# Optimization experiments

Measured on AMD Instinct MI355X. Metric: run time of the kernel, lower is better.

## Reference

```python
import jax, jax.numpy as jnp
import numpy as np
import math

N_COMP = 8          # config.project.shape[1]
REG_TOPK = 4        # config.reg_topk
PROJ_MAX = 7.0      # config.project = linspace(0, 7, 8)
ACC = PROJ_MAX / (N_COMP - 1)  # = 1.0


def _conv(x, w, b, pad):
    y = jax.lax.conv_general_dilated(
        x, w, window_strides=(1, 1), padding=[(pad, pad), (pad, pad)],
        dimension_numbers=("NCHW", "OIHW", "NCHW"))
    return y + b[None, :, None, None]


def setup_inputs() -> dict:
    key = jax.random.key(0)
    ks = jax.random.split(key, 16)
    std = 0.01
    f32 = jnp.float32
    feature = jax.random.normal(ks[0], (8, 256, 100, 152), dtype=f32)
    cls_w = jax.random.normal(ks[1], (4, 256, 256, 3, 3), dtype=f32) * std
    cls_b = jnp.zeros((4, 256), dtype=f32)
    box_w = jax.random.normal(ks[2], (4, 256, 256, 3, 3), dtype=f32) * std
    box_b = jnp.zeros((4, 256), dtype=f32)
    score_w = jax.random.normal(ks[3], (1, 256, 3, 3), dtype=f32) * std
    score_b = jnp.full((1,), -math.log((1 - 0.01) / 0.01), dtype=f32)
    pred_w = jax.random.normal(ks[4], (64, 256, 3, 3), dtype=f32) * std
    pred_b = jnp.zeros((64,), dtype=f32)
    ctn_w = jax.random.normal(ks[5], (1, 256, 3, 3), dtype=f32) * std
    ctn_b = jnp.zeros((1,), dtype=f32)
    conf_w1 = jax.random.normal(ks[6], (64, 48, 1, 1), dtype=f32) * std
    conf_b1 = jnp.zeros((64,), dtype=f32)
    conf_w2 = jax.random.normal(ks[7], (1, 64, 1, 1), dtype=f32) * std
    conf_b2 = jnp.zeros((1,), dtype=f32)
    return dict(feature=feature, cls_w=cls_w, cls_b=cls_b, box_w=box_w, box_b=box_b,
                score_w=score_w, score_b=score_b, pred_w=pred_w, pred_b=pred_b,
                ctn_w=ctn_w, ctn_b=ctn_b, conf_w1=conf_w1, conf_b1=conf_b1,
                conf_w2=conf_w2, conf_b2=conf_b2)


def reference(feature, cls_w, cls_b, box_w, box_b, score_w, score_b,
              pred_w, pred_b, ctn_w, ctn_b, conf_w1, conf_b1, conf_w2, conf_b2):
    x = feature
    for i in range(4):
        x = jax.nn.relu(_conv(x, cls_w[i], cls_b[i], 1))
    cls_score = _conv(x, score_w, score_b, 1)          # (N,1,H,W)
    # bbox subnet
    y = feature
    for i in range(4):
        y = jax.nn.relu(_conv(y, box_w[i], box_b[i], 1))
    bbox_pred = _conv(y, pred_w, pred_b, 1)            # (N,64,H,W)
    ctn = _conv(y, ctn_w, ctn_b, 1)                    # (N,1,H,W)

    N, C, H, W = bbox_pred.shape
    # rows = N*H*W*4 (4 box sides), 16 = 2*n_component per side
    flat = bbox_pred.transpose(0, 2, 3, 1).reshape(-1, 2 * N_COMP)
    logit = flat[:, :N_COMP]
    lstd = flat[:, N_COMP:]
    prob = jax.nn.softmax(logit, axis=1)               # (rows, n)
    sigma = jnp.exp(lstd)                              # (rows, n)
    proj = jnp.arange(N_COMP, dtype=flat.dtype) * ACC  # linspace(0, 7, 8)
    inv = 1.0 / (sigma * jnp.asarray(np.sqrt(2.0), flat.dtype))  # (rows, n)
    # Normal(mean=proj_i, std=sigma_i).cdf(proj_j +/- acc)
    diff = proj[None, None, :] - proj[None, :, None]   # (1, n_i, n_j) = z_j - mean_i
    cdf_hi = 0.5 * (1.0 + jax.lax.erf((diff + ACC) * inv[:, :, None]))
    cdf_lo = 0.5 * (1.0 + jax.lax.erf((diff - ACC) * inv[:, :, None]))
    pmf = jnp.sum((cdf_hi - cdf_lo) * prob[:, :, None], axis=1)  # (rows, n)

    toppmf, idx = jax.lax.top_k(pmf, REG_TOPK)         # (rows, k)
    toplstd = jnp.take_along_axis(lstd, idx, axis=1)
    topprob = jnp.take_along_axis(prob, idx, axis=1)

    def tochw(t):  # (rows,k) -> (N, 4*k, H, W)
        return t.reshape(N, H, W, -1).transpose(0, 3, 1, 2)

    stat = jnp.concatenate([tochw(toplstd), tochw(topprob), tochw(toppmf)], axis=1)  # (N,48,H,W)
    h = jax.nn.relu(_conv(stat, conf_w1, conf_b1, 0))
    quality = jax.nn.sigmoid(_conv(h, conf_w2, conf_b2, 0))  # (N,1,H,W)

    cls_out = jax.nn.sigmoid(cls_score) * quality
    pred_cls = cls_out.transpose(0, 2, 3, 1).reshape(N, -1, 1)
    pred_reg = bbox_pred.transpose(0, 2, 3, 1).reshape(N, -1, 4 * 2 * N_COMP)
    pred_ctn = ctn.transpose(0, 2, 3, 1).reshape(N, -1, 1)
    return (pred_cls, pred_reg, pred_ctn)
```

## Files before the change

kernel.cpp:

```cpp
#include <hip/hip_runtime.h>

typedef unsigned short u16;
typedef _Float16 f16;
typedef __attribute__((ext_vector_type(4))) float f32x4;
typedef __attribute__((ext_vector_type(8))) _Float16 f16x8;
typedef __attribute__((ext_vector_type(8))) unsigned short u16x8;

#define NIMG 8
#define HH 100
#define WW 152
#define HP 102
#define WP 154
#define NPIX (NIMG*HH*WW)
#define ACT_ELEMS ((size_t)NIMG*HP*WP*256)
#define ACT_BYTES (ACT_ELEMS*2)

__device__ __forceinline__ u16 f2h(float x){
    f16 h = (f16)x;
    return __builtin_bit_cast(u16, h);
}

__device__ __forceinline__ void g2l16(const u16* g, u16* l){
    __builtin_amdgcn_global_load_lds((const __attribute__((address_space(1))) unsigned int*)g,
                                     (__attribute__((address_space(3))) unsigned int*)l, 16, 0, 0);
}

__global__ void zero_borders(u16* A, u16* B){
    int id = blockIdx.x*256 + threadIdx.x;
    int ch = id & 31; int t = id >> 5;
    int pb = t % 508; int nimg = t / 508;
    int hp, wp;
    if (pb < 154)      { hp = 0;            wp = pb; }
    else if (pb < 308) { hp = 101;          wp = pb - 154; }
    else if (pb < 408) { hp = pb - 308 + 1; wp = 0; }
    else               { hp = pb - 408 + 1; wp = 153; }
    size_t off = ((size_t)((nimg*HP + hp)*WP + wp))*256 + ch*8;
    u16x8 z = {};
    *(u16x8*)(A+off) = z; *(u16x8*)(B+off) = z;
}

__global__ void feat2act(const float* __restrict__ F, u16* __restrict__ D){
    __shared__ float t[64][65];
    int bid = blockIdx.x;
    int wb = bid % 3; bid /= 3;
    int cb = bid & 3; bid >>= 2;
    int h = bid % 100; int nimg = bid / 100;
    int c0 = cb*64, w0 = wb*64;
    int tid = threadIdx.x;
    int cl = tid >> 6;
    int wl = tid & 63;
    #pragma unroll
    for (int rr=0; rr<16; ++rr){
        int c = rr*4 + cl;
        int w = w0 + wl;
        float v = 0.f;
        if (w < WW) v = F[ ((size_t)((nimg*256 + c0 + c)*HH + h))*WW + w ];
        t[c][wl] = v;
    }
    __syncthreads();
    int wl2 = tid >> 6;
    int cl2 = tid & 63;
    #pragma unroll
    for (int rr=0; rr<16; ++rr){
        int w = rr*4 + wl2;
        if (w0 + w < WW){
            size_t dst = ((size_t)((nimg*HP + h + 1)*WP + (w0 + w + 1)))*256 + c0 + cl2;
            D[dst] = f2h(t[cl2][w]);
        }
    }
}

__global__ void wt_tower(const float* __restrict__ src, u16* __restrict__ d){
    int idx = blockIdx.x*256 + threadIdx.x;
    int ci = idx & 255; int t = idx >> 8;
    int co = t & 255; t >>= 8;
    int tap = t % 9; int l = t / 9;
    d[idx] = f2h(src[ ((size_t)((l*256+co)*256+ci))*9 + tap ]);
}
__global__ void wt_predctn(const float* __restrict__ pw, const float* __restrict__ cw,
                           u16* __restrict__ d){
    int idx = blockIdx.x*256 + threadIdx.x;
    int ci = idx & 255; int co = (idx>>8) & 127; int tap = idx >> 15;
    float v = 0.f;
    if (co < 64)       v = pw[ ((size_t)(co*256+ci))*9 + tap ];
    else if (co == 64) v = cw[ (size_t)ci*9 + tap ];
    d[idx] = f2h(v);
}
__global__ void wt_score(const float* __restrict__ sw, u16* __restrict__ d){
    int idx = blockIdx.x*256 + threadIdx.x;
    int ci = idx & 255; int co = (idx>>8) & 127; int tap = idx >> 15;
    d[idx] = f2h((co == 0) ? sw[ (size_t)ci*9 + tap ] : 0.f);
}
__global__ void prep_bias(const float* pb, const float* cb, const float* sb, float* bpc, float* bsc){
    int i = threadIdx.x;
    bpc[i] = (i < 64) ? pb[i] : ((i == 64) ? cb[0] : 0.f);
    bsc[i] = (i == 0) ? sb[0] : 0.f;
}

template<int MODE>
__global__ __launch_bounds__(256, 2) void conv3x3_k(
    const u16* __restrict__ Ah, const u16* __restrict__ Wh,
    const float* __restrict__ bias,
    u16* __restrict__ Oh,
    float* __restrict__ O1, float* __restrict__ O2,
    int NB, int COUTP)
{
    __shared__ u16 lds[32768];
    const int tid  = threadIdx.x;
    const int lane = tid & 63;
    const int wave = tid >> 6;

    int nwg = gridDim.x;
    int bid = blockIdx.x;
    int qq  = nwg >> 3;
    int swz = (bid & 7)*qq + (bid >> 3);
    int nblk = swz % NB;
    int mblk = swz / NB;
    int nimg = mblk / 125;
    int rem  = mblk - nimg*125;
    int ht   = rem / 5;
    int wt5  = rem - ht*5;
    int h0 = ht*4, w0 = wt5*32;
    int co0 = nblk*128;

    int aoff[4], boff[4];
    #pragma unroll
    for (int it=0; it<4; ++it){
        int s = it*256 + tid;
        int p = s >> 3, ch = s & 7;
        int chs = ch ^ (p & 7);
        int i = p >> 5, j = p & 31;
        aoff[it] = ((nimg*HP + h0 + i)*WP + (w0 + j))*256 + chs*8;
        boff[it] = (co0 + p)*256 + chs*8;
    }
    const int ldst = wave*512;

    const int r  = lane & 15;
    const int q4 = lane >> 4;
    const int c0k = ((q4    ) ^ (r & 7)) * 8;
    const int c1k = ((q4 + 4) ^ (r & 7)) * 8;
    const int wm = wave >> 1, wn = wave & 1;
    const int aBase = (wm*64 + r)*64;
    const int bBase = 8192 + (wn*64 + r)*64;

    f32x4 acc[4][4];
    #pragma unroll
    for (int m=0;m<4;m++)
        #pragma unroll
        for (int n=0;n<4;n++)
            acc[m][n] = (f32x4)0.0f;

    auto stage = [&](int t, int b){
        int tap = t >> 2, kb = t & 3;
        int kh = tap/3, kw = tap - kh*3;
        int adel = (kh*WP + kw)*256 + kb*64;
        int bdel = tap*COUTP*256 + kb*64;
        u16* L = lds + b*16384;
        #pragma unroll
        for (int it=0; it<4; ++it)
            g2l16(Ah + aoff[it] + adel, L +        it*2048 + ldst);
        #pragma unroll
        for (int it=0; it<4; ++it)
            g2l16(Wh + boff[it] + bdel, L + 8192 + it*2048 + ldst);
    };

    stage(0, 0);
    stage(1, 1);
    asm volatile("s_waitcnt vmcnt(8)" ::: "memory");
    __builtin_amdgcn_s_barrier();

    for (int t=0; t<36; ++t){
        int b = t & 1;
        const u16* L = lds + b*16384;
        f16x8 a0[4], a1[4], b0[4], b1[4];
        #pragma unroll
        for (int m=0;m<4;m++){
            a0[m] = *(const f16x8*)(L + aBase + m*1024 + c0k);
            a1[m] = *(const f16x8*)(L + aBase + m*1024 + c1k);
            b0[m] = *(const f16x8*)(L + bBase + m*1024 + c0k);
            b1[m] = *(const f16x8*)(L + bBase + m*1024 + c1k);
        }
        asm volatile("s_waitcnt lgkmcnt(0)" ::: "memory");
        __builtin_amdgcn_s_barrier();
        __builtin_amdgcn_sched_barrier(0);
        if (t < 34) stage(t+2, b);
        __builtin_amdgcn_s_setprio(1);
        #pragma unroll
        for (int n=0;n<4;n++){
            #pragma unroll
            for (int m=0;m<4;m++){
                acc[m][n] = __builtin_amdgcn_mfma_f32_16x16x32_f16(a0[m], b0[n], acc[m][n], 0,0,0);
                acc[m][n] = __builtin_amdgcn_mfma_f32_16x16x32_f16(a1[m], b1[n], acc[m][n], 0,0,0);
            }
        }
        __builtin_amdgcn_s_setprio(0);
        __builtin_amdgcn_sched_barrier(0);
        if (t < 34) { asm volatile("s_waitcnt vmcnt(8)" ::: "memory"); }
        else        { asm volatile("s_waitcnt vmcnt(0)" ::: "memory"); }
        __builtin_amdgcn_s_barrier();
    }

    float bcol[4];
    #pragma unroll
    for (int n=0;n<4;n++) bcol[n] = bias[co0 + wn*64 + n*16 + r];

    if (MODE == 0){
        #pragma unroll
        for (int m=0;m<4;m++)
            #pragma unroll
            for (int n=0;n<4;n++)
                #pragma unroll
                for (int jj=0;jj<4;jj++){
                    float v = fmaxf(acc[m][n][jj] + bcol[n], 0.f);
                    int p = wm*64 + m*16 + q4*4 + jj;
                    int c = wn*64 + n*16 + r;
                    lds[p*128 + c] = f2h(v);
                }
        __syncthreads();
        #pragma unroll
        for (int it=0; it<8; ++it){
            int s = it*256 + tid;
            int p = s >> 4, chh = s & 15;
            int i = p >> 5, j = p & 31;
            if (w0 + j < WW){
                size_t dst = ((size_t)((nimg*HP + h0 + i + 1)*WP + (w0 + j + 1)))*256 + co0 + chh*8;
                *(u16x8*)(Oh + dst) = *(const u16x8*)(lds + p*128 + chh*8);
            }
        }
    } else {
        #pragma unroll
        for (int m=0;m<4;m++)
            #pragma unroll
            for (int n=0;n<4;n++)
                #pragma unroll
                for (int jj=0;jj<4;jj++){
                    float v = acc[m][n][jj] + bcol[n];
                    int p = wm*64 + m*16 + q4*4 + jj;
                    int c = co0 + wn*64 + n*16 + r;
                    int i = p >> 5, j = p & 31;
                    if (w0 + j < WW){
                        int pix = nimg*(HH*WW) + (h0+i)*WW + (w0+j);
                        if (MODE == 1){
                            if (c < 64)       O1[(size_t)pix*64 + c] = v;
                            else if (c == 64) O2[pix] = v;
                        } else {
                            if (c == 0) O1[pix] = v;
                        }
                    }
                }
    }
}

__global__ __launch_bounds__(256) void fuse_stat(
    const float* __restrict__ bbox, const float* __restrict__ cls_score,
    const float* __restrict__ w1, const float* __restrict__ b1,
    const float* __restrict__ w2, const float* __restrict__ b2,
    float* __restrict__ pred_cls)
{
    __shared__ float sstat[48][256];
    int tid = threadIdx.x;
    int pix = blockIdx.x*256 + tid;
    if (pix >= NPIX) return;
    const f32x4* row4 = (const f32x4*)(bbox + (size_t)pix*64);
    for (int g=0; g<4; ++g){
        f32x4 v0 = row4[g*4+0], v1 = row4[g*4+1], v2 = row4[g*4+2], v3 = row4[g*4+3];
        float lg[8], ls[8];
        #pragma unroll
        for (int k=0;k<4;k++){ lg[k]=v0[k]; lg[4+k]=v1[k]; ls[k]=v2[k]; ls[4+k]=v3[k]; }
        float m = lg[0];
        #pragma unroll
        for (int k=1;k<8;k++) m = fmaxf(m, lg[k]);
        float e[8], s = 0.f;
        #pragma unroll
        for (int k=0;k<8;k++){ e[k] = expf(lg[k]-m); s += e[k]; }
        float isum = 1.0f/s;
        float prob[8];
        #pragma unroll
        for (int k=0;k<8;k++) prob[k] = e[k]*isum;
        float pmf[8];
        #pragma unroll
        for (int k=0;k<8;k++) pmf[k] = 0.f;
        #pragma unroll
        for (int i=0;i<8;i++){
            float invi = 1.0f/(expf(ls[i]) * 1.41421356237309515f);
            float pi = prob[i];
            #pragma unroll
            for (int j=0;j<8;j++){
                float d = (float)(j - i);
                pmf[j] = fmaf(0.5f*(erff((d+1.0f)*invi) - erff((d-1.0f)*invi)), pi, pmf[j]);
            }
        }
        int used = 0;
        #pragma unroll
        for (int t=0;t<4;t++){
            float bv = -3.0e38f; int bi = 0;
            #pragma unroll
            for (int j=0;j<8;j++){
                bool ok = (((used>>j)&1)==0) && (pmf[j] > bv);
                bv = ok ? pmf[j] : bv;
                bi = ok ? j : bi;
            }
            used |= (1<<bi);
            float sl=0.f, sp=0.f;
            #pragma unroll
            for (int j=0;j<8;j++){ if (j==bi){ sl=ls[j]; sp=prob[j]; } }
            sstat[g*4+t][tid]    = sl;
            sstat[16+g*4+t][tid] = sp;
            sstat[32+g*4+t][tid] = bv;
        }
    }
    float q = b2[0];
    for (int u=0; u<64; ++u){
        float h = b1[u];
        #pragma unroll
        for (int c=0;c<48;c++) h = fmaf(sstat[c][tid], w1[u*48+c], h);
        q = fmaf(fmaxf(h,0.f), w2[u], q);
    }
    float quality = 1.0f/(1.0f+expf(-q));
    float cs = cls_score[pix];
    pred_cls[pix] = quality/(1.0f+expf(-cs));
}

extern "C" void kernel_launch(void* const* d_in, const int* in_sizes, int n_in,
                              void* d_out, int out_size, void* d_ws, size_t ws_size,
                              hipStream_t stream) {
    (void)in_sizes; (void)n_in; (void)out_size;
    const float* feature = (const float*)d_in[0];
    const float* cls_w   = (const float*)d_in[1];
    const float* cls_b   = (const float*)d_in[2];
    const float* box_w   = (const float*)d_in[3];
    const float* box_b   = (const float*)d_in[4];
    const float* score_w = (const float*)d_in[5];
    const float* score_b = (const float*)d_in[6];
    const float* pred_w  = (const float*)d_in[7];
    const float* pred_b  = (const float*)d_in[8];
    const float* ctn_w   = (const float*)d_in[9];
    const float* ctn_b   = (const float*)d_in[10];
    const float* conf_w1 = (const float*)d_in[11];
    const float* conf_b1 = (const float*)d_in[12];
    const float* conf_w2 = (const float*)d_in[13];
    const float* conf_b2 = (const float*)d_in[14];

    float* out      = (float*)d_out;
    float* pred_cls = out;
    float* pred_reg = out + NPIX;
    float* pred_ctn = out + NPIX + (size_t)NPIX*64;

    char* ws = (char*)d_ws;
    size_t off = 0;
    auto alloc = [&](size_t b){ size_t rr = off; off += (b + 255) & ~(size_t)255; return rr; };
    u16* aA = (u16*)(ws + alloc(ACT_BYTES));
    u16* aB = (u16*)(ws + alloc(ACT_BYTES));
    const size_t TWR = (size_t)4*9*256*256;
    const size_t HDW = (size_t)9*128*256;
    u16* wCls = (u16*)(ws + alloc(TWR*2));
    u16* wBox = (u16*)(ws + alloc(TWR*2));
    u16* wSc  = (u16*)(ws + alloc(HDW*2));
    u16* wPc  = (u16*)(ws + alloc(HDW*2));
    float* bPc = (float*)(ws + alloc(128*4));
    float* bSc = (float*)(ws + alloc(128*4));
    float* clsScore = (float*)(ws + alloc((size_t)NPIX*4));
    if (ws_size < off) return;

    dim3 B(256);
    zero_borders<<<508, B, 0, stream>>>(aA, aB);
    wt_tower<<<9216, B, 0, stream>>>(cls_w, wCls);
    wt_tower<<<9216, B, 0, stream>>>(box_w, wBox);
    wt_score<<<1152, B, 0, stream>>>(score_w, wSc);
    wt_predctn<<<1152, B, 0, stream>>>(pred_w, ctn_w, wPc);
    prep_bias<<<1, 128, 0, stream>>>(pred_b, ctn_b, score_b, bPc, bSc);

    const size_t LW = (size_t)9*256*256;
    feat2act<<<9600, B, 0, stream>>>(feature, aA);
    conv3x3_k<0><<<2000, B, 0, stream>>>(aA, wCls+0*LW, cls_b+0*256, aB, nullptr, nullptr, 2, 256);
    conv3x3_k<0><<<2000, B, 0, stream>>>(aB, wCls+1*LW, cls_b+1*256, aA, nullptr, nullptr, 2, 256);
    conv3x3_k<0><<<2000, B, 0, stream>>>(aA, wCls+2*LW, cls_b+2*256, aB, nullptr, nullptr, 2, 256);
    conv3x3_k<0><<<2000, B, 0, stream>>>(aB, wCls+3*LW, cls_b+3*256, aA, nullptr, nullptr, 2, 256);
    conv3x3_k<2><<<1000, B, 0, stream>>>(aA, wSc, bSc, nullptr, clsScore, nullptr, 1, 128);
    feat2act<<<9600, B, 0, stream>>>(feature, aB);
    conv3x3_k<0><<<2000, B, 0, stream>>>(aB, wBox+0*LW, box_b+0*256, aA, nullptr, nullptr, 2, 256);
    conv3x3_k<0><<<2000, B, 0, stream>>>(aA, wBox+1*LW, box_b+1*256, aB, nullptr, nullptr, 2, 256);
    conv3x3_k<0><<<2000, B, 0, stream>>>(aB, wBox+2*LW, box_b+2*256, aA, nullptr, nullptr, 2, 256);
    conv3x3_k<0><<<2000, B, 0, stream>>>(aA, wBox+3*LW, box_b+3*256, aB, nullptr, nullptr, 2, 256);
    conv3x3_k<1><<<1000, B, 0, stream>>>(aB, wPc, bPc, nullptr, pred_reg, pred_ctn, 1, 128);
    fuse_stat<<<475, B, 0, stream>>>(pred_reg, clsScore, conf_w1, conf_b1, conf_w2, conf_b2, pred_cls);
}
```

Baseline: 1.420 ms.

## Load conv weights straight to registers and trim padded head output channels

The conv kernel no longer stages weight tiles through LDS. Each wave now loads its B fragments from global memory into registers, double-buffered a step ahead. The head convolutions get specialised tiling: 16 output channels for the score head and 80 for pred+ctn instead of 128, with each wave covering 32 pixels, which cuts the wasted MFMA work on padded channels. LDS use halves, but the tower convs now read weights redundantly per wave from global or L2, adding register pressure and load latency on the main path.

```diff
diff --git a/kernel.cpp b/kernel.cpp
--- a/kernel.cpp
+++ b/kernel.cpp
@@ -80,7 +80,8 @@
 __global__ void wt_predctn(const float* __restrict__ pw, const float* __restrict__ cw,
                            u16* __restrict__ d){
     int idx = blockIdx.x*256 + threadIdx.x;
-    int ci = idx & 255; int co = (idx>>8) & 127; int tap = idx >> 15;
+    int ci = idx & 255; int t = idx >> 8;
+    int co = t % 80; int tap = t / 80;
     float v = 0.f;
     if (co < 64)       v = pw[ ((size_t)(co*256+ci))*9 + tap ];
     else if (co == 64) v = cw[ (size_t)ci*9 + tap ];
@@ -88,7 +89,8 @@
 }
 __global__ void wt_score(const float* __restrict__ sw, u16* __restrict__ d){
     int idx = blockIdx.x*256 + threadIdx.x;
-    int ci = idx & 255; int co = (idx>>8) & 127; int tap = idx >> 15;
+    int ci = idx & 255; int t = idx >> 8;
+    int co = t & 15; int tap = t >> 4;
     d[idx] = f2h((co == 0) ? sw[ (size_t)ci*9 + tap ] : 0.f);
 }
 __global__ void prep_bias(const float* pb, const float* cb, const float* sb, float* bpc, float* bsc){
@@ -99,13 +101,17 @@
 
 template<int MODE>
 __global__ __launch_bounds__(256, 2) void conv3x3_k(
-    const u16* __restrict__ Ah, const u16* __restrict__ Wh,
+    const u16* __restrict__ Ain, const u16* __restrict__ W,
     const float* __restrict__ bias,
     u16* __restrict__ Oh,
     float* __restrict__ O1, float* __restrict__ O2,
     int NB, int COUTP)
 {
-    __shared__ u16 lds[32768];
+    constexpr int MR = (MODE==0) ? 4 : 2;
+    constexpr int NR = (MODE==0) ? 4 : ((MODE==1) ? 5 : 1);
+    constexpr int VMN = 4 + 2*NR;
+
+    __shared__ u16 lds[16384];
     const int tid  = threadIdx.x;
     const int lane = tid & 63;
     const int wave = tid >> 6;
@@ -121,9 +127,8 @@
     int ht   = rem / 5;
     int wt5  = rem - ht*5;
     int h0 = ht*4, w0 = wt5*32;
-    int co0 = nblk*128;
-
-    int aoff[4], boff[4];
+
+    int aoff[4];
     #pragma unroll
     for (int it=0; it<4; ++it){
         int s = it*256 + tid;
@@ -131,7 +136,6 @@
         int chs = ch ^ (p & 7);
         int i = p >> 5, j = p & 31;
         aoff[it] = ((nimg*HP + h0 + i)*WP + (w0 + j))*256 + chs*8;
-        boff[it] = (co0 + p)*256 + chs*8;
     }
     const int ldst = wave*512;
 
@@ -139,76 +143,92 @@
     const int q4 = lane >> 4;
     const int c0k = ((q4    ) ^ (r & 7)) * 8;
     const int c1k = ((q4 + 4) ^ (r & 7)) * 8;
-    const int wm = wave >> 1, wn = wave & 1;
-    const int aBase = (wm*64 + r)*64;
-    const int bBase = 8192 + (wn*64 + r)*64;
-
-    f32x4 acc[4][4];
-    #pragma unroll
-    for (int m=0;m<4;m++)
-        #pragma unroll
-        for (int n=0;n<4;n++)
+    int wm, wn;
+    if (MODE == 0){ wm = wave >> 1; wn = wave & 1; } else { wm = wave; wn = 0; }
+    const int aBase = (wm*(MR*16) + r)*64;
+    const int cobase = (MODE==0) ? (nblk*128 + wn*64) : 0;
+
+    int bvo[NR];
+    #pragma unroll
+    for (int n=0;n<NR;n++) bvo[n] = (cobase + n*16 + r)*256 + q4*8;
+
+    f32x4 acc[MR][NR];
+    #pragma unroll
+    for (int m=0;m<MR;m++)
+        #pragma unroll
+        for (int n=0;n<NR;n++)
             acc[m][n] = (f32x4)0.0f;
 
     auto stage = [&](int t, int b){
         int tap = t >> 2, kb = t & 3;
         int kh = tap/3, kw = tap - kh*3;
         int adel = (kh*WP + kw)*256 + kb*64;
-        int bdel = tap*COUTP*256 + kb*64;
-        u16* L = lds + b*16384;
+        u16* L = lds + b*8192;
         #pragma unroll
         for (int it=0; it<4; ++it)
-            g2l16(Ah + aoff[it] + adel, L +        it*2048 + ldst);
-        #pragma unroll
-        for (int it=0; it<4; ++it)
-            g2l16(Wh + boff[it] + bdel, L + 8192 + it*2048 + ldst);
+            g2l16(Ain + aoff[it] + adel, L + it*2048 + ldst);
     };
+    auto loadB = [&](int t, f16x8 (&d)[NR][2]){
+        int tap = t >> 2, kb = t & 3;
+        int base = tap*COUTP*256 + kb*64;
+        #pragma unroll
+        for (int n=0;n<NR;n++){
+            d[n][0] = *(const f16x8*)(W + base + bvo[n]);
+            d[n][1] = *(const f16x8*)(W + base + bvo[n] + 32);
+        }
+    };
+
+    f16x8 bA[NR][2], bB[NR][2];
 
     stage(0, 0);
     stage(1, 1);
-    asm volatile("s_waitcnt vmcnt(8)" ::: "memory");
+    loadB(0, bA);
+    asm volatile("s_waitcnt vmcnt(%0)" :: "i"(VMN) : "memory");
     __builtin_amdgcn_s_barrier();
 
-    for (int t=0; t<36; ++t){
-        int b = t & 1;
-        const u16* L = lds + b*16384;
-        f16x8 a0[4], a1[4], b0[4], b1[4];
-        #pragma unroll
-        for (int m=0;m<4;m++){
-            a0[m] = *(const f16x8*)(L + aBase + m*1024 + c0k);
-            a1[m] = *(const f16x8*)(L + aBase + m*1024 + c1k);
-            b0[m] = *(const f16x8*)(L + bBase + m*1024 + c0k);
-            b1[m] = *(const f16x8*)(L + bBase + m*1024 + c1k);
+    auto step = [&](int t, int b, f16x8 (&use)[NR][2], f16x8 (&nxt)[NR][2]){
+        const u16* L = lds + b*8192;
+        f16x8 af[MR][2];
+        #pragma unroll
+        for (int m=0;m<MR;m++){
+            af[m][0] = *(const f16x8*)(L + aBase + m*1024 + c0k);
+            af[m][1] = *(const f16x8*)(L + aBase + m*1024 + c1k);
         }
         asm volatile("s_waitcnt lgkmcnt(0)" ::: "memory");
         __builtin_amdgcn_s_barrier();
         __builtin_amdgcn_sched_barrier(0);
         if (t < 34) stage(t+2, b);
+        if (t < 35) loadB(t+1, nxt);
         __builtin_amdgcn_s_setprio(1);
         #pragma unroll
-        for (int n=0;n<4;n++){
-            #pragma unroll
-            for (int m=0;m<4;m++){
-                acc[m][n] = __builtin_amdgcn_mfma_f32_16x16x32_f16(a0[m], b0[n], acc[m][n], 0,0,0);
-                acc[m][n] = __builtin_amdgcn_mfma_f32_16x16x32_f16(a1[m], b1[n], acc[m][n], 0,0,0);
+        for (int n=0;n<NR;n++){
+            #pragma unroll
+            for (int m=0;m<MR;m++){
+                acc[m][n] = __builtin_amdgcn_mfma_f32_16x16x32_f16(af[m][0], use[n][0], acc[m][n], 0,0,0);
+                acc[m][n] = __builtin_amdgcn_mfma_f32_16x16x32_f16(af[m][1], use[n][1], acc[m][n], 0,0,0);
             }
         }
         __builtin_amdgcn_s_setprio(0);
         __builtin_amdgcn_sched_barrier(0);
-        if (t < 34) { asm volatile("s_waitcnt vmcnt(8)" ::: "memory"); }
-        else        { asm volatile("s_waitcnt vmcnt(0)" ::: "memory"); }
+        asm volatile("s_waitcnt vmcnt(%0)" :: "i"(VMN) : "memory");
         __builtin_amdgcn_s_barrier();
-    }
-
-    float bcol[4];
-    #pragma unroll
-    for (int n=0;n<4;n++) bcol[n] = bias[co0 + wn*64 + n*16 + r];
+    };
+
+    #pragma unroll 1
+    for (int tt=0; tt<36; tt+=2){
+        step(tt,   0, bA, bB);
+        step(tt+1, 1, bB, bA);
+    }
+
+    float bcol[NR];
+    #pragma unroll
+    for (int n=0;n<NR;n++) bcol[n] = bias[cobase + n*16 + r];
 
     if (MODE == 0){
         #pragma unroll
-        for (int m=0;m<4;m++)
-            #pragma unroll
-            for (int n=0;n<4;n++)
+        for (int m=0;m<MR;m++)
+            #pragma unroll
+            for (int n=0;n<NR;n++)
                 #pragma unroll
                 for (int jj=0;jj<4;jj++){
                     float v = fmaxf(acc[m][n][jj] + bcol[n], 0.f);
@@ -223,20 +243,20 @@
             int p = s >> 4, chh = s & 15;
             int i = p >> 5, j = p & 31;
             if (w0 + j < WW){
-                size_t dst = ((size_t)((nimg*HP + h0 + i + 1)*WP + (w0 + j + 1)))*256 + co0 + chh*8;
+                size_t dst = ((size_t)((nimg*HP + h0 + i + 1)*WP + (w0 + j + 1)))*256 + nblk*128 + chh*8;
                 *(u16x8*)(Oh + dst) = *(const u16x8*)(lds + p*128 + chh*8);
             }
         }
     } else {
         #pragma unroll
-        for (int m=0;m<4;m++)
-            #pragma unroll
-            for (int n=0;n<4;n++)
+        for (int m=0;m<MR;m++)
+            #pragma unroll
+            for (int n=0;n<NR;n++)
                 #pragma unroll
                 for (int jj=0;jj<4;jj++){
                     float v = acc[m][n][jj] + bcol[n];
-                    int p = wm*64 + m*16 + q4*4 + jj;
-                    int c = co0 + wn*64 + n*16 + r;
+                    int p = wm*32 + m*16 + q4*4 + jj;
+                    int c = n*16 + r;
                     int i = p >> 5, j = p & 31;
                     if (w0 + j < WW){
                         int pix = nimg*(HH*WW) + (h0+i)*WW + (w0+j);
@@ -352,11 +372,10 @@
     u16* aA = (u16*)(ws + alloc(ACT_BYTES));
     u16* aB = (u16*)(ws + alloc(ACT_BYTES));
     const size_t TWR = (size_t)4*9*256*256;
-    const size_t HDW = (size_t)9*128*256;
     u16* wCls = (u16*)(ws + alloc(TWR*2));
     u16* wBox = (u16*)(ws + alloc(TWR*2));
-    u16* wSc  = (u16*)(ws + alloc(HDW*2));
-    u16* wPc  = (u16*)(ws + alloc(HDW*2));
+    u16* wSc  = (u16*)(ws + alloc((size_t)9*16*256*2));
+    u16* wPc  = (u16*)(ws + alloc((size_t)9*80*256*2));
     float* bPc = (float*)(ws + alloc(128*4));
     float* bSc = (float*)(ws + alloc(128*4));
     float* clsScore = (float*)(ws + alloc((size_t)NPIX*4));
@@ -366,8 +385,8 @@
     zero_borders<<<508, B, 0, stream>>>(aA, aB);
     wt_tower<<<9216, B, 0, stream>>>(cls_w, wCls);
     wt_tower<<<9216, B, 0, stream>>>(box_w, wBox);
-    wt_score<<<1152, B, 0, stream>>>(score_w, wSc);
-    wt_predctn<<<1152, B, 0, stream>>>(pred_w, ctn_w, wPc);
+    wt_score<<<144, B, 0, stream>>>(score_w, wSc);
+    wt_predctn<<<720, B, 0, stream>>>(pred_w, ctn_w, wPc);
     prep_bias<<<1, 128, 0, stream>>>(pred_b, ctn_b, score_b, bPc, bSc);
 
     const size_t LW = (size_t)9*256*256;
@@ -376,12 +395,12 @@
     conv3x3_k<0><<<2000, B, 0, stream>>>(aB, wCls+1*LW, cls_b+1*256, aA, nullptr, nullptr, 2, 256);
     conv3x3_k<0><<<2000, B, 0, stream>>>(aA, wCls+2*LW, cls_b+2*256, aB, nullptr, nullptr, 2, 256);
     conv3x3_k<0><<<2000, B, 0, stream>>>(aB, wCls+3*LW, cls_b+3*256, aA, nullptr, nullptr, 2, 256);
-    conv3x3_k<2><<<1000, B, 0, stream>>>(aA, wSc, bSc, nullptr, clsScore, nullptr, 1, 128);
+    conv3x3_k<2><<<1000, B, 0, stream>>>(aA, wSc, bSc, nullptr, clsScore, nullptr, 1, 16);
     feat2act<<<9600, B, 0, stream>>>(feature, aB);
     conv3x3_k<0><<<2000, B, 0, stream>>>(aB, wBox+0*LW, box_b+0*256, aA, nullptr, nullptr, 2, 256);
     conv3x3_k<0><<<2000, B, 0, stream>>>(aA, wBox+1*LW, box_b+1*256, aB, nullptr, nullptr, 2, 256);
     conv3x3_k<0><<<2000, B, 0, stream>>>(aB, wBox+2*LW, box_b+2*256, aA, nullptr, nullptr, 2, 256);
     conv3x3_k<0><<<2000, B, 0, stream>>>(aA, wBox+3*LW, box_b+3*256, aB, nullptr, nullptr, 2, 256);
-    conv3x3_k<1><<<1000, B, 0, stream>>>(aB, wPc, bPc, nullptr, pred_reg, pred_ctn, 1, 128);
+    conv3x3_k<1><<<1000, B, 0, stream>>>(aB, wPc, bPc, nullptr, pred_reg, pred_ctn, 1, 80);
     fuse_stat<<<475, B, 0, stream>>>(pred_reg, clsScore, conf_w1, conf_b1, conf_w2, conf_b2, pred_cls);
 }
```

After: 2.864 ms. +101.7%, slower.

## Load a shared halo tile once per channel block and reuse it across taps

Applied to the files above, without the earlier changes.

The 3x3 conv kernel now stages a 10x34-pixel halo of activations into LDS once per 64-channel block and reads all nine tap windows from it, instead of reloading a shifted activation tile from global memory for every tap. Each workgroup grows to 512 threads covering 8x32 output pixels, and only the weight tiles stay double-buffered per tap. The aim is to cut redundant activation traffic and issue fewer global-to-LDS loads per MFMA. In exchange, LDS use per block rises, the grid wastes some work on the partial last row of tiles, rows are clamped at the bottom, and the activation buffers get extra slack space to absorb reads past the end.

```diff
diff --git a/kernel.cpp b/kernel.cpp
--- a/kernel.cpp
+++ b/kernel.cpp
@@ -14,6 +14,10 @@
 #define NPIX (NIMG*HH*WW)
 #define ACT_ELEMS ((size_t)NIMG*HP*WP*256)
 #define ACT_BYTES (ACT_ELEMS*2)
+
+#define HALO_U16 22528
+#define BBUF_U16 8192
+#define LDS_U16  38912
 
 __device__ __forceinline__ u16 f2h(float x){
     f16 h = (f16)x;
@@ -98,14 +102,13 @@
 }
 
 template<int MODE>
-__global__ __launch_bounds__(256, 2) void conv3x3_k(
-    const u16* __restrict__ Ah, const u16* __restrict__ Wh,
+__global__ __launch_bounds__(512, 2) void conv3x3_k(
+    const u16* __restrict__ Ain, const u16* __restrict__ W,
     const float* __restrict__ bias,
-    u16* __restrict__ Oh,
-    float* __restrict__ O1, float* __restrict__ O2,
+    u16* __restrict__ Oh, float* __restrict__ O1, float* __restrict__ O2,
     int NB, int COUTP)
 {
-    __shared__ u16 lds[32768];
+    __shared__ u16 lds[LDS_U16];
     const int tid  = threadIdx.x;
     const int lane = tid & 63;
     const int wave = tid >> 6;
@@ -116,32 +119,39 @@
     int swz = (bid & 7)*qq + (bid >> 3);
     int nblk = swz % NB;
     int mblk = swz / NB;
-    int nimg = mblk / 125;
-    int rem  = mblk - nimg*125;
+    int nimg = mblk / 65;
+    int rem  = mblk - nimg*65;
     int ht   = rem / 5;
     int wt5  = rem - ht*5;
-    int h0 = ht*4, w0 = wt5*32;
+    int h0 = ht*8, w0 = wt5*32;
     int co0 = nblk*128;
 
-    int aoff[4], boff[4];
-    #pragma unroll
-    for (int it=0; it<4; ++it){
-        int s = it*256 + tid;
+    int hsrc[6];
+    #pragma unroll
+    for (int it=0; it<6; ++it){
+        int s = it*512 + tid;
         int p = s >> 3, ch = s & 7;
         int chs = ch ^ (p & 7);
-        int i = p >> 5, j = p & 31;
-        aoff[it] = ((nimg*HP + h0 + i)*WP + (w0 + j))*256 + chs*8;
-        boff[it] = (co0 + p)*256 + chs*8;
-    }
-    const int ldst = wave*512;
+        int hh = p / 34, ww = p - hh*34;
+        int row = h0 + hh; if (row > 101) row = 101;
+        hsrc[it] = ((nimg*HP + row)*WP + (w0 + ww))*256 + chs*8;
+    }
+    int bsrc[2];
+    #pragma unroll
+    for (int it=0; it<2; ++it){
+        int s = it*512 + tid;
+        int p = s >> 3, ch = s & 7;
+        int chs = ch ^ (p & 7);
+        bsrc[it] = (co0 + p)*256 + chs*8;
+    }
+    const int wofs = wave*512;
 
     const int r  = lane & 15;
     const int q4 = lane >> 4;
-    const int c0k = ((q4    ) ^ (r & 7)) * 8;
-    const int c1k = ((q4 + 4) ^ (r & 7)) * 8;
-    const int wm = wave >> 1, wn = wave & 1;
-    const int aBase = (wm*64 + r)*64;
-    const int bBase = 8192 + (wn*64 + r)*64;
+    const int mg = wave >> 1;
+    const int wn = wave & 1;
+    const int laneHBase = mg*68 + r;
+    const int bRead = (wn*64 + r)*64 + (q4 ^ (r & 7))*8;
 
     f32x4 acc[4][4];
     #pragma unroll
@@ -150,52 +160,75 @@
         for (int n=0;n<4;n++)
             acc[m][n] = (f32x4)0.0f;
 
-    auto stage = [&](int t, int b){
-        int tap = t >> 2, kb = t & 3;
-        int kh = tap/3, kw = tap - kh*3;
-        int adel = (kh*WP + kw)*256 + kb*64;
-        int bdel = tap*COUTP*256 + kb*64;
-        u16* L = lds + b*16384;
-        #pragma unroll
-        for (int it=0; it<4; ++it)
-            g2l16(Ah + aoff[it] + adel, L +        it*2048 + ldst);
-        #pragma unroll
-        for (int it=0; it<4; ++it)
-            g2l16(Wh + boff[it] + bdel, L + 8192 + it*2048 + ldst);
+    auto stageHalo = [&](int kb){
+        int kofs = kb*64;
+        u16* L = lds + wofs;
+        #pragma unroll
+        for (int it=0; it<5; ++it)
+            g2l16(Ain + hsrc[it] + kofs, L + it*4096);
+        if (tid < 160) g2l16(Ain + hsrc[5] + kofs, L + 5*4096);
     };
-
-    stage(0, 0);
-    stage(1, 1);
-    asm volatile("s_waitcnt vmcnt(8)" ::: "memory");
+    auto stageB = [&](int tap2, int kb2, int buf){
+        int wb = tap2*COUTP*256 + kb2*64;
+        u16* L = lds + HALO_U16 + buf*BBUF_U16 + wofs;
+        #pragma unroll
+        for (int it=0; it<2; ++it)
+            g2l16(W + wb + bsrc[it], L + it*4096);
+    };
+
+    stageHalo(0);
+    stageB(0, 0, 0);
+    stageB(1, 0, 1);
+    asm volatile("s_waitcnt vmcnt(2)" ::: "memory");
     __builtin_amdgcn_s_barrier();
 
+    #pragma unroll 1
     for (int t=0; t<36; ++t){
-        int b = t & 1;
-        const u16* L = lds + b*16384;
-        f16x8 a0[4], a1[4], b0[4], b1[4];
-        #pragma unroll
-        for (int m=0;m<4;m++){
-            a0[m] = *(const f16x8*)(L + aBase + m*1024 + c0k);
-            a1[m] = *(const f16x8*)(L + aBase + m*1024 + c1k);
-            b0[m] = *(const f16x8*)(L + bBase + m*1024 + c0k);
-            b1[m] = *(const f16x8*)(L + bBase + m*1024 + c1k);
+        int kb  = t/9;
+        int tap = t - kb*9;
+        int kh  = tap/3;
+        int kw  = tap - kh*3;
+        int hp  = laneHBase + kh*34 + kw;
+        int aA  = hp*64  + (q4 ^ (hp  & 7))*8;
+        int hp2 = hp + 34;
+        int aB  = hp2*64 + (q4 ^ (hp2 & 7))*8;
+        const u16* Lb = lds + HALO_U16 + (t & 1)*BBUF_U16;
+
+        f16x8 af[4][2], bf[4][2];
+        af[0][0] = *(const f16x8*)(lds + aA);
+        af[0][1] = *(const f16x8*)(lds + (aA ^ 32));
+        af[1][0] = *(const f16x8*)(lds + aA + 1024);
+        af[1][1] = *(const f16x8*)(lds + (aA ^ 32) + 1024);
+        af[2][0] = *(const f16x8*)(lds + aB);
+        af[2][1] = *(const f16x8*)(lds + (aB ^ 32));
+        af[3][0] = *(const f16x8*)(lds + aB + 1024);
+        af[3][1] = *(const f16x8*)(lds + (aB ^ 32) + 1024);
+        #pragma unroll
+        for (int n=0;n<4;n++){
+            bf[n][0] = *(const f16x8*)(Lb + bRead + n*1024);
+            bf[n][1] = *(const f16x8*)(Lb + (bRead ^ 32) + n*1024);
         }
         asm volatile("s_waitcnt lgkmcnt(0)" ::: "memory");
         __builtin_amdgcn_s_barrier();
         __builtin_amdgcn_sched_barrier(0);
-        if (t < 34) stage(t+2, b);
+        if (tap == 8 && kb < 3) stageHalo(kb+1);
+        if (t < 34){
+            int tn = t + 2;
+            int kbn = tn/9;
+            stageB(tn - kbn*9, kbn, t & 1);
+        }
         __builtin_amdgcn_s_setprio(1);
         #pragma unroll
         for (int n=0;n<4;n++){
             #pragma unroll
             for (int m=0;m<4;m++){
-                acc[m][n] = __builtin_amdgcn_mfma_f32_16x16x32_f16(a0[m], b0[n], acc[m][n], 0,0,0);
-                acc[m][n] = __builtin_amdgcn_mfma_f32_16x16x32_f16(a1[m], b1[n], acc[m][n], 0,0,0);
+                acc[m][n] = __builtin_amdgcn_mfma_f32_16x16x32_f16(af[m][0], bf[n][0], acc[m][n], 0,0,0);
+                acc[m][n] = __builtin_amdgcn_mfma_f32_16x16x32_f16(af[m][1], bf[n][1], acc[m][n], 0,0,0);
             }
         }
         __builtin_amdgcn_s_setprio(0);
         __builtin_amdgcn_sched_barrier(0);
-        if (t < 34) { asm volatile("s_waitcnt vmcnt(8)" ::: "memory"); }
+        if (t < 34) { asm volatile("s_waitcnt vmcnt(2)" ::: "memory"); }
         else        { asm volatile("s_waitcnt vmcnt(0)" ::: "memory"); }
         __builtin_amdgcn_s_barrier();
     }
@@ -212,19 +245,19 @@
                 #pragma unroll
                 for (int jj=0;jj<4;jj++){
                     float v = fmaxf(acc[m][n][jj] + bcol[n], 0.f);
-                    int p = wm*64 + m*16 + q4*4 + jj;
+                    int p = mg*64 + m*16 + q4*4 + jj;
                     int c = wn*64 + n*16 + r;
-                    lds[p*128 + c] = f2h(v);
+                    lds[p*132 + c] = f2h(v);
                 }
         __syncthreads();
         #pragma unroll
         for (int it=0; it<8; ++it){
-            int s = it*256 + tid;
+            int s = it*512 + tid;
             int p = s >> 4, chh = s & 15;
             int i = p >> 5, j = p & 31;
-            if (w0 + j < WW){
+            if (h0 + i < HH && w0 + j < WW){
                 size_t dst = ((size_t)((nimg*HP + h0 + i + 1)*WP + (w0 + j + 1)))*256 + co0 + chh*8;
-                *(u16x8*)(Oh + dst) = *(const u16x8*)(lds + p*128 + chh*8);
+                *(u16x8*)(Oh + dst) = *(const u16x8*)(lds + p*132 + chh*8);
             }
         }
     } else {
@@ -235,10 +268,10 @@
                 #pragma unroll
                 for (int jj=0;jj<4;jj++){
                     float v = acc[m][n][jj] + bcol[n];
-                    int p = wm*64 + m*16 + q4*4 + jj;
-                    int c = co0 + wn*64 + n*16 + r;
+                    int p = mg*64 + m*16 + q4*4 + jj;
+                    int c = wn*64 + n*16 + r;
                     int i = p >> 5, j = p & 31;
-                    if (w0 + j < WW){
+                    if (h0 + i < HH && w0 + j < WW){
                         int pix = nimg*(HH*WW) + (h0+i)*WW + (w0+j);
                         if (MODE == 1){
                             if (c < 64)       O1[(size_t)pix*64 + c] = v;
@@ -349,8 +382,8 @@
     char* ws = (char*)d_ws;
     size_t off = 0;
     auto alloc = [&](size_t b){ size_t rr = off; off += (b + 255) & ~(size_t)255; return rr; };
-    u16* aA = (u16*)(ws + alloc(ACT_BYTES));
-    u16* aB = (u16*)(ws + alloc(ACT_BYTES));
+    u16* aA = (u16*)(ws + alloc(ACT_BYTES + 65536));
+    u16* aB = (u16*)(ws + alloc(ACT_BYTES + 65536));
     const size_t TWR = (size_t)4*9*256*256;
     const size_t HDW = (size_t)9*128*256;
     u16* wCls = (u16*)(ws + alloc(TWR*2));
@@ -371,17 +404,18 @@
     prep_bias<<<1, 128, 0, stream>>>(pred_b, ctn_b, score_b, bPc, bSc);
 
     const size_t LW = (size_t)9*256*256;
+    dim3 CB(512);
     feat2act<<<9600, B, 0, stream>>>(feature, aA);
-    conv3x3_k<0><<<2000, B, 0, stream>>>(aA, wCls+0*LW, cls_b+0*256, aB, nullptr, nullptr, 2, 256);
-    conv3x3_k<0><<<2000, B, 0, stream>>>(aB, wCls+1*LW, cls_b+1*256, aA, nullptr, nullptr, 2, 256);
-    conv3x3_k<0><<<2000, B, 0, stream>>>(aA, wCls+2*LW, cls_b+2*256, aB, nullptr, nullptr, 2, 256);
-    conv3x3_k<0><<<2000, B, 0, stream>>>(aB, wCls+3*LW, cls_b+3*256, aA, nullptr, nullptr, 2, 256);
-    conv3x3_k<2><<<1000, B, 0, stream>>>(aA, wSc, bSc, nullptr, clsScore, nullptr, 1, 128);
+    conv3x3_k<0><<<1040, CB, 0, stream>>>(aA, wCls+0*LW, cls_b+0*256, aB, nullptr, nullptr, 2, 256);
+    conv3x3_k<0><<<1040, CB, 0, stream>>>(aB, wCls+1*LW, cls_b+1*256, aA, nullptr, nullptr, 2, 256);
+    conv3x3_k<0><<<1040, CB, 0, stream>>>(aA, wCls+2*LW, cls_b+2*256, aB, nullptr, nullptr, 2, 256);
+    conv3x3_k<0><<<1040, CB, 0, stream>>>(aB, wCls+3*LW, cls_b+3*256, aA, nullptr, nullptr, 2, 256);
+    conv3x3_k<2><<<520, CB, 0, stream>>>(aA, wSc, bSc, nullptr, clsScore, nullptr, 1, 128);
     feat2act<<<9600, B, 0, stream>>>(feature, aB);
-    conv3x3_k<0><<<2000, B, 0, stream>>>(aB, wBox+0*LW, box_b+0*256, aA, nullptr, nullptr, 2, 256);
-    conv3x3_k<0><<<2000, B, 0, stream>>>(aA, wBox+1*LW, box_b+1*256, aB, nullptr, nullptr, 2, 256);
-    conv3x3_k<0><<<2000, B, 0, stream>>>(aB, wBox+2*LW, box_b+2*256, aA, nullptr, nullptr, 2, 256);
-    conv3x3_k<0><<<2000, B, 0, stream>>>(aA, wBox+3*LW, box_b+3*256, aB, nullptr, nullptr, 2, 256);
-    conv3x3_k<1><<<1000, B, 0, stream>>>(aB, wPc, bPc, nullptr, pred_reg, pred_ctn, 1, 128);
+    conv3x3_k<0><<<1040, CB, 0, stream>>>(aB, wBox+0*LW, box_b+0*256, aA, nullptr, nullptr, 2, 256);
+    conv3x3_k<0><<<1040, CB, 0, stream>>>(aA, wBox+1*LW, box_b+1*256, aB, nullptr, nullptr, 2, 256);
+    conv3x3_k<0><<<1040, CB, 0, stream>>>(aB, wBox+2*LW, box_b+2*256, aA, nullptr, nullptr, 2, 256);
+    conv3x3_k<0><<<1040, CB, 0, stream>>>(aA, wBox+3*LW, box_b+3*256, aB, nullptr, nullptr, 2, 256);
+    conv3x3_k<1><<<520, CB, 0, stream>>>(aB, wPc, bPc, nullptr, pred_reg, pred_ctn, 1, 128);
     fuse_stat<<<475, B, 0, stream>>>(pred_reg, clsScore, conf_w1, conf_b1, conf_w2, conf_b2, pred_cls);
 }
```

Result: slower. 1.957 ms (+37.9%).

## Batch cls and box tower convs into joint launches; trim head MFMA tiles

Applied to the files above, without the earlier changes.

The cls and box towers now run together: each tower layer is one 4000-block launch whose blocks pick cls or box operands by index, using four activation buffers instead of two. Feature conversion writes both tower inputs in a single pass, and the weight transposes are merged into one launch. The head convs (score and pred/ctn) use narrower accumulator tiles (1 or 5 column fragments instead of 4) so padded output channels are not computed. The intent is to cut launch count, fill the GPU better in each launch and drop wasted MFMA work in the heads, at the cost of doubled activation workspace.

```diff
diff --git a/kernel.cpp b/kernel.cpp
--- a/kernel.cpp
+++ b/kernel.cpp
@@ -25,7 +25,7 @@
                                      (__attribute__((address_space(3))) unsigned int*)l, 16, 0, 0);
 }
 
-__global__ void zero_borders(u16* A, u16* B){
+__global__ void zero_borders(u16* A, u16* B, u16* C, u16* D){
     int id = blockIdx.x*256 + threadIdx.x;
     int ch = id & 31; int t = id >> 5;
     int pb = t % 508; int nimg = t / 508;
@@ -37,9 +37,10 @@
     size_t off = ((size_t)((nimg*HP + hp)*WP + wp))*256 + ch*8;
     u16x8 z = {};
     *(u16x8*)(A+off) = z; *(u16x8*)(B+off) = z;
-}
-
-__global__ void feat2act(const float* __restrict__ F, u16* __restrict__ D){
+    *(u16x8*)(C+off) = z; *(u16x8*)(D+off) = z;
+}
+
+__global__ void feat2act(const float* __restrict__ F, u16* __restrict__ D1, u16* __restrict__ D2){
     __shared__ float t[64][65];
     int bid = blockIdx.x;
     int wb = bid % 3; bid /= 3;
@@ -64,14 +65,21 @@
     for (int rr=0; rr<16; ++rr){
         int w = rr*4 + wl2;
         if (w0 + w < WW){
+            u16 h16 = f2h(t[cl2][w]);
             size_t dst = ((size_t)((nimg*HP + h + 1)*WP + (w0 + w + 1)))*256 + c0 + cl2;
-            D[dst] = f2h(t[cl2][w]);
-        }
-    }
-}
-
-__global__ void wt_tower(const float* __restrict__ src, u16* __restrict__ d){
-    int idx = blockIdx.x*256 + threadIdx.x;
+            D1[dst] = h16;
+            D2[dst] = h16;
+        }
+    }
+}
+
+__global__ void wt_tower(const float* __restrict__ srcC, const float* __restrict__ srcB,
+                         u16* __restrict__ dC, u16* __restrict__ dB){
+    int gidx = blockIdx.x*256 + threadIdx.x;
+    const int HALF = 4*9*256*256;
+    const float* src = (gidx < HALF) ? srcC : srcB;
+    u16* d           = (gidx < HALF) ? dC : dB;
+    int idx = (gidx < HALF) ? gidx : gidx - HALF;
     int ci = idx & 255; int t = idx >> 8;
     int co = t & 255; t >>= 8;
     int tap = t % 9; int l = t / 9;
@@ -99,12 +107,16 @@
 
 template<int MODE>
 __global__ __launch_bounds__(256, 2) void conv3x3_k(
-    const u16* __restrict__ Ah, const u16* __restrict__ Wh,
-    const float* __restrict__ bias,
-    u16* __restrict__ Oh,
+    const u16* __restrict__ Ain0, const u16* __restrict__ Ain1,
+    const u16* __restrict__ W0,  const u16* __restrict__ W1,
+    const float* __restrict__ bias0, const float* __restrict__ bias1,
+    u16* __restrict__ Oh0, u16* __restrict__ Oh1,
     float* __restrict__ O1, float* __restrict__ O2,
-    int NB, int COUTP)
+    int nPerTower, int NB, int COUTP)
 {
+    constexpr int MR = (MODE==0) ? 4 : 2;
+    constexpr int NR = (MODE==0) ? 4 : ((MODE==1) ? 5 : 1);
+
     __shared__ u16 lds[32768];
     const int tid  = threadIdx.x;
     const int lane = tid & 63;
@@ -114,8 +126,16 @@
     int bid = blockIdx.x;
     int qq  = nwg >> 3;
     int swz = (bid & 7)*qq + (bid >> 3);
-    int nblk = swz % NB;
-    int mblk = swz / NB;
+    int tower = (swz >= nPerTower) ? 1 : 0;
+    int id = swz - tower*nPerTower;
+
+    const u16* Ain    = tower ? Ain1  : Ain0;
+    const u16* W      = tower ? W1    : W0;
+    const float* bias = tower ? bias1 : bias0;
+    u16* Oh           = tower ? Oh1   : Oh0;
+
+    int nblk = id % NB;
+    int mblk = id / NB;
     int nimg = mblk / 125;
     int rem  = mblk - nimg*125;
     int ht   = rem / 5;
@@ -139,15 +159,16 @@
     const int q4 = lane >> 4;
     const int c0k = ((q4    ) ^ (r & 7)) * 8;
     const int c1k = ((q4 + 4) ^ (r & 7)) * 8;
-    const int wm = wave >> 1, wn = wave & 1;
-    const int aBase = (wm*64 + r)*64;
+    int wm, wn;
+    if (MODE == 0){ wm = wave >> 1; wn = wave & 1; } else { wm = wave; wn = 0; }
+    const int aBase = (wm*(MR*16) + r)*64;
     const int bBase = 8192 + (wn*64 + r)*64;
 
-    f32x4 acc[4][4];
+    f32x4 acc[MR][NR];
     #pragma unroll
-    for (int m=0;m<4;m++)
-        #pragma unroll
-        for (int n=0;n<4;n++)
+    for (int m=0;m<MR;m++)
+        #pragma unroll
+        for (int n=0;n<NR;n++)
             acc[m][n] = (f32x4)0.0f;
 
     auto stage = [&](int t, int b){
@@ -158,10 +179,10 @@
         u16* L = lds + b*16384;
         #pragma unroll
         for (int it=0; it<4; ++it)
-            g2l16(Ah + aoff[it] + adel, L +        it*2048 + ldst);
+            g2l16(Ain + aoff[it] + adel, L +        it*2048 + ldst);
         #pragma unroll
         for (int it=0; it<4; ++it)
-            g2l16(Wh + boff[it] + bdel, L + 8192 + it*2048 + ldst);
+            g2l16(W + bdel + boff[it], L + 8192 + it*2048 + ldst);
     };
 
     stage(0, 0);
@@ -172,13 +193,16 @@
     for (int t=0; t<36; ++t){
         int b = t & 1;
         const u16* L = lds + b*16384;
-        f16x8 a0[4], a1[4], b0[4], b1[4];
-        #pragma unroll
-        for (int m=0;m<4;m++){
+        f16x8 a0[MR], a1[MR], b0[NR], b1[NR];
+        #pragma unroll
+        for (int m=0;m<MR;m++){
             a0[m] = *(const f16x8*)(L + aBase + m*1024 + c0k);
             a1[m] = *(const f16x8*)(L + aBase + m*1024 + c1k);
-            b0[m] = *(const f16x8*)(L + bBase + m*1024 + c0k);
-            b1[m] = *(const f16x8*)(L + bBase + m*1024 + c1k);
+        }
+        #pragma unroll
+        for (int n=0;n<NR;n++){
+            b0[n] = *(const f16x8*)(L + bBase + n*1024 + c0k);
+            b1[n] = *(const f16x8*)(L + bBase + n*1024 + c1k);
         }
         asm volatile("s_waitcnt lgkmcnt(0)" ::: "memory");
         __builtin_amdgcn_s_barrier();
@@ -186,9 +210,9 @@
         if (t < 34) stage(t+2, b);
         __builtin_amdgcn_s_setprio(1);
         #pragma unroll
-        for (int n=0;n<4;n++){
-            #pragma unroll
-            for (int m=0;m<4;m++){
+        for (int n=0;n<NR;n++){
+            #pragma unroll
+            for (int m=0;m<MR;m++){
                 acc[m][n] = __builtin_amdgcn_mfma_f32_16x16x32_f16(a0[m], b0[n], acc[m][n], 0,0,0);
                 acc[m][n] = __builtin_amdgcn_mfma_f32_16x16x32_f16(a1[m], b1[n], acc[m][n], 0,0,0);
             }
@@ -200,15 +224,15 @@
         __builtin_amdgcn_s_barrier();
     }
 
-    float bcol[4];
+    float bcol[NR];
     #pragma unroll
-    for (int n=0;n<4;n++) bcol[n] = bias[co0 + wn*64 + n*16 + r];
+    for (int n=0;n<NR;n++) bcol[n] = bias[co0 + wn*64 + n*16 + r];
 
     if (MODE == 0){
         #pragma unroll
-        for (int m=0;m<4;m++)
-            #pragma unroll
-            for (int n=0;n<4;n++)
+        for (int m=0;m<MR;m++)
+            #pragma unroll
+            for (int n=0;n<NR;n++)
                 #pragma unroll
                 for (int jj=0;jj<4;jj++){
                     float v = fmaxf(acc[m][n][jj] + bcol[n], 0.f);
@@ -229,14 +253,14 @@
         }
     } else {
         #pragma unroll
-        for (int m=0;m<4;m++)
-            #pragma unroll
-            for (int n=0;n<4;n++)
+        for (int m=0;m<MR;m++)
+            #pragma unroll
+            for (int n=0;n<NR;n++)
                 #pragma unroll
                 for (int jj=0;jj<4;jj++){
                     float v = acc[m][n][jj] + bcol[n];
-                    int p = wm*64 + m*16 + q4*4 + jj;
-                    int c = co0 + wn*64 + n*16 + r;
+                    int p = wm*32 + m*16 + q4*4 + jj;
+                    int c = n*16 + r;
                     int i = p >> 5, j = p & 31;
                     if (w0 + j < WW){
                         int pix = nimg*(HH*WW) + (h0+i)*WW + (w0+j);
@@ -349,8 +373,10 @@
     char* ws = (char*)d_ws;
     size_t off = 0;
     auto alloc = [&](size_t b){ size_t rr = off; off += (b + 255) & ~(size_t)255; return rr; };
-    u16* aA = (u16*)(ws + alloc(ACT_BYTES));
-    u16* aB = (u16*)(ws + alloc(ACT_BYTES));
+    u16* aA = (u16*)(ws + alloc(ACT_BYTES + 65536));
+    u16* aB = (u16*)(ws + alloc(ACT_BYTES + 65536));
+    u16* aC = (u16*)(ws + alloc(ACT_BYTES + 65536));
+    u16* aD = (u16*)(ws + alloc(ACT_BYTES + 65536));
     const size_t TWR = (size_t)4*9*256*256;
     const size_t HDW = (size_t)9*128*256;
     u16* wCls = (u16*)(ws + alloc(TWR*2));
@@ -363,25 +389,19 @@
     if (ws_size < off) return;
 
     dim3 B(256);
-    zero_borders<<<508, B, 0, stream>>>(aA, aB);
-    wt_tower<<<9216, B, 0, stream>>>(cls_w, wCls);
-    wt_tower<<<9216, B, 0, stream>>>(box_w, wBox);
+    zero_borders<<<508, B, 0, stream>>>(aA, aB, aC, aD);
+    wt_tower<<<18432, B, 0, stream>>>(cls_w, box_w, wCls, wBox);
     wt_score<<<1152, B, 0, stream>>>(score_w, wSc);
     wt_predctn<<<1152, B, 0, stream>>>(pred_w, ctn_w, wPc);
     prep_bias<<<1, 128, 0, stream>>>(pred_b, ctn_b, score_b, bPc, bSc);
 
     const size_t LW = (size_t)9*256*256;
-    feat2act<<<9600, B, 0, stream>>>(feature, aA);
-    conv3x3_k<0><<<2000, B, 0, stream>>>(aA, wCls+0*LW, cls_b+0*256, aB, nullptr, nullptr, 2, 256);
-    conv3x3_k<0><<<2000, B, 0, stream>>>(aB, wCls+1*LW, cls_b+1*256, aA, nullptr, nullptr, 2, 256);
-    conv3x3_k<0><<<2000, B, 0, stream>>>(aA, wCls+2*LW, cls_b+2*256, aB, nullptr, nullptr, 2, 256);
-    conv3x3_k<0><<<2000, B, 0, stream>>>(aB, wCls+3*LW, cls_b+3*256, aA, nullptr, nullptr, 2, 256);
-    conv3x3_k<2><<<1000, B, 0, stream>>>(aA, wSc, bSc, nullptr, clsScore, nullptr, 1, 128);
-    feat2act<<<9600, B, 0, stream>>>(feature, aB);
-    conv3x3_k<0><<<2000, B, 0, stream>>>(aB, wBox+0*LW, box_b+0*256, aA, nullptr, nullptr, 2, 256);
-    conv3x3_k<0><<<2000, B, 0, stream>>>(aA, wBox+1*LW, box_b+1*256, aB, nullptr, nullptr, 2, 256);
-    conv3x3_k<0><<<2000, B, 0, stream>>>(aB, wBox+2*LW, box_b+2*256, aA, nullptr, nullptr, 2, 256);
-    conv3x3_k<0><<<2000, B, 0, stream>>>(aA, wBox+3*LW, box_b+3*256, aB, nullptr, nullptr, 2, 256);
-    conv3x3_k<1><<<1000, B, 0, stream>>>(aB, wPc, bPc, nullptr, pred_reg, pred_ctn, 1, 128);
+    feat2act<<<9600, B, 0, stream>>>(feature, aA, aC);
+    conv3x3_k<0><<<4000, B, 0, stream>>>(aA, aC, wCls+0*LW, wBox+0*LW, cls_b+0*256, box_b+0*256, aB, aD, nullptr, nullptr, 2000, 2, 256);
+    conv3x3_k<0><<<4000, B, 0, stream>>>(aB, aD, wCls+1*LW, wBox+1*LW, cls_b+1*256, box_b+1*256, aA, aC, nullptr, nullptr, 2000, 2, 256);
+    conv3x3_k<0><<<4000, B, 0, stream>>>(aA, aC, wCls+2*LW, wBox+2*LW, cls_b+2*256, box_b+2*256, aB, aD, nullptr, nullptr, 2000, 2, 256);
+    conv3x3_k<0><<<4000, B, 0, stream>>>(aB, aD, wCls+3*LW, wBox+3*LW, cls_b+3*256, box_b+3*256, aA, aC, nullptr, nullptr, 2000, 2, 256);
+    conv3x3_k<2><<<1000, B, 0, stream>>>(aA, aA, wSc, wSc, bSc, bSc, nullptr, nullptr, clsScore, nullptr, 1000, 1, 128);
+    conv3x3_k<1><<<1000, B, 0, stream>>>(aC, aC, wPc, wPc, bPc, bPc, nullptr, nullptr, pred_reg, pred_ctn, 1000, 1, 128);
     fuse_stat<<<475, B, 0, stream>>>(pred_reg, clsScore, conf_w1, conf_b1, conf_w2, conf_b2, pred_cls);
 }
```

After: 1.357 ms. 1.05x faster.
